# Performance work log

Measured on AMD Instinct MI355X. Metric: run time of the kernel, lower is better.

The kernel has to match this reference:

```python
import jax, jax.numpy as jnp
import numpy as np

FREQ = 129  # STFT_FILTERS // 2


def conv1d(x, w, b, stride, pad):
    # x: [B, Cin, L], w: [Cout, Cin, K] (torch Conv1d layout)
    out = jax.lax.conv_general_dilated(x, w, (stride,), [(pad, pad)],
                                       dimension_numbers=('NCH', 'OIH', 'NCH'))
    if b is not None:
        out = out + b[None, :, None]
    return out


def setup_inputs() -> dict:
    key = jax.random.key(0)
    ks = jax.random.split(key, 17)
    B = 16384
    s = 0.05
    return {
        'x': jax.random.normal(ks[0], (B, 512), jnp.float32),
        'state': jax.random.normal(ks[1], (2, B, 128), jnp.float32),
        'stft_w': jax.random.normal(ks[2], (258, 1, 256), jnp.float32) * s,
        'w1': jax.random.normal(ks[3], (128, 129, 3), jnp.float32) * s,
        'b1': jax.random.normal(ks[4], (128,), jnp.float32) * s,
        'w2': jax.random.normal(ks[5], (64, 128, 3), jnp.float32) * s,
        'b2': jax.random.normal(ks[6], (64,), jnp.float32) * s,
        'w3': jax.random.normal(ks[7], (64, 64, 3), jnp.float32) * s,
        'b3': jax.random.normal(ks[8], (64,), jnp.float32) * s,
        'w4': jax.random.normal(ks[9], (128, 64, 3), jnp.float32) * s,
        'b4': jax.random.normal(ks[10], (128,), jnp.float32) * s,
        'w_ih': jax.random.normal(ks[11], (512, 128), jnp.float32) * s,
        'w_hh': jax.random.normal(ks[12], (512, 128), jnp.float32) * s,
        'b_ih': jax.random.normal(ks[13], (512,), jnp.float32) * s,
        'b_hh': jax.random.normal(ks[14], (512,), jnp.float32) * s,
        'fw': jax.random.normal(ks[15], (1, 128, 1), jnp.float32) * s,
        'fb': jax.random.normal(ks[16], (1,), jnp.float32) * s,
    }


def reference(x, state, stft_w, w1, b1, w2, b2, w3, b3, w4, b4,
              w_ih, w_hh, b_ih, b_hh, fw, fb):
    # reflect-pad right by 64: [B, 512] -> [B, 576], add channel dim
    xp = jnp.pad(x, ((0, 0), (0, 64)), mode='reflect')[:, None, :]
    s = conv1d(xp, stft_w, None, 128, 0)            # [B, 258, 3]
    real, imag = s[:, :FREQ], s[:, FREQ:]
    h = jnp.sqrt(real * real + imag * imag)          # magnitude [B, 129, 3]
    h = jax.nn.relu(conv1d(h, w1, b1, 1, 1))         # [B, 128, 3]
    h = jax.nn.relu(conv1d(h, w2, b2, 2, 1))         # [B, 64, 2]
    h = jax.nn.relu(conv1d(h, w3, b3, 2, 1))         # [B, 64, 1]
    h = jax.nn.relu(conv1d(h, w4, b4, 1, 1))         # [B, 128, 1]
    feat = h[:, :, 0]                                # [B, 128]
    # torch LSTMCell: gate order i, f, g, o
    gates = feat @ w_ih.T + b_ih + state[0] @ w_hh.T + b_hh
    i, f, g, o = jnp.split(gates, 4, axis=1)
    c = jax.nn.sigmoid(f) * state[1] + jax.nn.sigmoid(i) * jnp.tanh(g)
    hn = jax.nn.sigmoid(o) * jnp.tanh(c)
    new_state = jnp.stack([hn, c], axis=0)           # [2, B, 128]
    z = jax.nn.relu(hn)[:, :, None]                  # [B, 128, 1]
    z = jax.nn.sigmoid(conv1d(z, fw, fb, 1, 0))      # [B, 1, 1]
    out = z[:, 0].mean(axis=1, keepdims=True)        # [B, 1]
    return out, new_state
```

## Files before the change

kernel.cpp:

```cpp
#include <hip/hip_runtime.h>
#include <math.h>

typedef unsigned short ushort_t;
typedef short short8 __attribute__((ext_vector_type(8)));
typedef float floatx4 __attribute__((ext_vector_type(4)));

#define MFMA16(a,b,c) __builtin_amdgcn_mfma_f32_16x16x32_bf16((a),(b),(c),0,0,0)

#define PK_STFT 0
#define PK_W1   69632
#define PK_W2   131072
#define PK_W3   155648
#define PK_W4   167936
#define PK_LSTM 176128
#define OFF_MAG 307200
#define OFF_FEAT 8171520

__device__ __forceinline__ ushort_t f2bf(float f){
    unsigned int u = __float_as_uint(f);
    u += 0x7fffu + ((u >> 16) & 1u);
    return (ushort_t)(u >> 16);
}
__device__ __forceinline__ float bf2f(ushort_t h){
    return __uint_as_float(((unsigned int)h) << 16);
}
__device__ __forceinline__ unsigned int pack2(float a, float b){
    return (unsigned int)f2bf(a) | ((unsigned int)f2bf(b) << 16);
}
__device__ __forceinline__ float sigf(float v){ return 1.f / (1.f + expf(-v)); }

__global__ __launch_bounds__(256) void prep_kernel(
    const float* __restrict__ stft_w, const float* __restrict__ w1,
    const float* __restrict__ w2, const float* __restrict__ w3,
    const float* __restrict__ w4, const float* __restrict__ wih,
    const float* __restrict__ whh, ushort_t* __restrict__ wp)
{
    int i = blockIdx.x * 256 + threadIdx.x;
    if (i >= 307200) return;
    float val = 0.f;
    if (i < PK_W1) {
        int frag = i >> 9, rr = i & 511, l = rr >> 3, j = rr & 7;
        int ct = frag >> 3, kk = frag & 7;
        int kd = kk * 32 + ((l >> 4) << 3) + j;
        int n = ct * 16 + (l & 15);
        val = (n < 258) ? stft_w[n * 256 + kd] : 0.f;
    } else if (i < PK_W2) {
        int r = i - PK_W1;
        int tap = r / 20480; r -= tap * 20480;
        int frag = r >> 9, rr = r & 511, l = rr >> 3, j = rr & 7;
        int ct = frag / 5, kk = frag - ct * 5;
        int kd = kk * 32 + ((l >> 4) << 3) + j;
        int c = ct * 16 + (l & 15);
        val = (kd < 129) ? w1[c * 387 + kd * 3 + tap] : 0.f;
    } else if (i < PK_W3) {
        int r = i - PK_W2;
        int frag = r >> 9, rr = r & 511, l = rr >> 3, j = rr & 7;
        int ct = frag / 12, kk = frag - ct * 12;
        int kd = kk * 32 + ((l >> 4) << 3) + j;
        int k = kd >> 7, f = kd & 127;
        int c = ct * 16 + (l & 15);
        val = w2[c * 384 + f * 3 + k];
    } else if (i < PK_W4) {
        int r = i - PK_W3;
        int frag = r >> 9, rr = r & 511, l = rr >> 3, j = rr & 7;
        int ct = frag / 6, kk = frag - ct * 6;
        int kd = kk * 32 + ((l >> 4) << 3) + j;
        int k = kd >> 6, f = kd & 63;
        int c = ct * 16 + (l & 15);
        val = w3[c * 192 + f * 3 + k];
    } else if (i < PK_LSTM) {
        int r = i - PK_W4;
        int frag = r >> 9, rr = r & 511, l = rr >> 3, j = rr & 7;
        int ct = frag >> 1, kk = frag & 1;
        int kd = kk * 32 + ((l >> 4) << 3) + j;
        int c = ct * 16 + (l & 15);
        val = w4[c * 192 + kd * 3 + 1];
    } else {
        int r = i - PK_LSTM;
        int frag = r >> 9, rr = r & 511, l = rr >> 3, j = rr & 7;
        int ct = frag >> 3, kk = frag & 7;
        int kd = kk * 32 + ((l >> 4) << 3) + j;
        int n = ct * 16 + (l & 15);
        val = (kd < 128) ? wih[n * 128 + kd] : whh[n * 128 + (kd - 128)];
    }
    wp[i] = f2bf(val);
}

__global__ __launch_bounds__(256) void stft_kernel(
    const float* __restrict__ x, const ushort_t* __restrict__ wp,
    ushort_t* __restrict__ magg)
{
    __shared__ ushort_t xs[48 * 264];
    __shared__ ushort_t s[48 * 264];
    const int tid = threadIdx.x, lane = tid & 63, wid = tid >> 6;
    const int l15 = lane & 15, lk = lane >> 4;

    {
        const float4* xg = (const float4*)(x + (size_t)blockIdx.x * 16 * 512);
#pragma unroll
        for (int i = 0; i < 8; ++i) {
            int idx4 = tid + i * 256;
            float4 v = xg[idx4];
            int b = idx4 >> 7, c4 = idx4 & 127;
            int si = c4 * 4, t1 = si >> 7;
            unsigned int u0 = pack2(v.x, v.y), u1 = pack2(v.z, v.w);
            if (t1 < 3) {
                ushort_t* p = &xs[(b * 3 + t1) * 264 + (si & 127)];
                *(unsigned int*)p = u0; *(unsigned int*)(p + 2) = u1;
            }
            if (t1 >= 1) {
                ushort_t* p = &xs[(b * 3 + t1 - 1) * 264 + (si & 127) + 128];
                *(unsigned int*)p = u0; *(unsigned int*)(p + 2) = u1;
            }
        }
    }
    __syncthreads();

    for (int ct = wid; ct < 17; ct += 4) {
        short8 bfrag[8];
        const short8* bp = (const short8*)(wp + PK_STFT) + (size_t)(ct * 8) * 64 + lane;
#pragma unroll
        for (int kk = 0; kk < 8; ++kk) bfrag[kk] = bp[kk * 64];
        int col = ct * 16 + l15;
#pragma unroll
        for (int rt = 0; rt < 3; ++rt) {
            const ushort_t* abase = &xs[(rt * 16 + l15) * 264 + lk * 8];
            floatx4 acc = {0.f, 0.f, 0.f, 0.f};
#pragma unroll
            for (int kk = 0; kk < 8; ++kk) {
                short8 af = *(const short8*)(abase + kk * 32);
                acc = MFMA16(af, bfrag[kk], acc);
            }
            if (col < 258) {
                int r0 = rt * 16 + lk * 4;
#pragma unroll
                for (int jj = 0; jj < 4; ++jj) s[(r0 + jj) * 264 + col] = f2bf(acc[jj]);
            }
        }
    }
    __syncthreads();

    {
        size_t ob = (size_t)blockIdx.x * 16 * 480;
        for (int idx = tid; idx < 48 * 129; idx += 256) {
            int bt = idx / 129, f = idx - bt * 129;
            float re = bf2f(s[bt * 264 + f]);
            float im = bf2f(s[bt * 264 + 129 + f]);
            int b = bt / 3, t = bt - b * 3;
            magg[ob + b * 480 + t * 160 + f] = f2bf(sqrtf(re * re + im * im));
        }
        for (int idx = tid; idx < 48 * 31; idx += 256) {
            int bt = idx / 31, f = 129 + (idx - bt * 31);
            int b = bt / 3, t = bt - b * 3;
            magg[ob + b * 480 + t * 160 + f] = 0;
        }
    }
}

__global__ __launch_bounds__(256) void conv_kernel(
    const ushort_t* __restrict__ wp, const ushort_t* __restrict__ magg,
    const float* __restrict__ b1, const float* __restrict__ b2,
    const float* __restrict__ b3, const float* __restrict__ b4,
    ushort_t* __restrict__ featg)
{
    __shared__ ushort_t big[26880];
    __shared__ ushort_t h2h[32 * 3 * 72];
    __shared__ ushort_t h3s[32 * 72];
    const int tid = threadIdx.x, lane = tid & 63, wid = tid >> 6;
    const int l15 = lane & 15, lk = lane >> 4;

    {
        unsigned int* bz = (unsigned int*)big;
        for (int i = tid; i < 5376; i += 256) {
            int bb = i / 168, r = i - bb * 168;
            int tp = (r < 84) ? 0 : 4, f2 = (r < 84) ? r : r - 84;
            bz[(bb * 5 + tp) * 84 + f2] = 0u;
        }
        for (int i = tid; i < 32 * 36; i += 256) {
            int bb = i / 36, f2 = i - bb * 36;
            ((unsigned int*)h2h)[bb * 108 + f2] = 0u;
        }
        const unsigned int* mg = (const unsigned int*)(magg + (size_t)blockIdx.x * 32 * 480);
        for (int i = tid; i < 7680; i += 256) {
            int bb = i / 240, r = i - bb * 240;
            int t = r / 80, f2 = r - t * 80;
            bz[(bb * 5 + 1 + t) * 84 + f2] = mg[i];
        }
    }
    __syncthreads();

    floatx4 acc1[2][6];
#pragma unroll
    for (int ci = 0; ci < 2; ++ci)
#pragma unroll
        for (int rt = 0; rt < 6; ++rt) acc1[ci][rt] = (floatx4){0.f, 0.f, 0.f, 0.f};
#pragma unroll
    for (int ci = 0; ci < 2; ++ci) {
        int ct = wid + ci * 4;
        short8 bfrag[15];
#pragma unroll
        for (int tap = 0; tap < 3; ++tap)
#pragma unroll
            for (int kk = 0; kk < 5; ++kk)
                bfrag[tap * 5 + kk] = ((const short8*)(wp + PK_W1))[(size_t)(tap * 40 + ct * 5 + kk) * 64 + lane];
#pragma unroll
        for (int rt = 0; rt < 6; ++rt) {
            int obt = rt * 16 + l15;
            int b = obt / 3, t = obt - b * 3;
#pragma unroll
            for (int tap = 0; tap < 3; ++tap) {
                const ushort_t* abase = &big[(b * 5 + t + tap) * 168 + lk * 8];
#pragma unroll
                for (int kk = 0; kk < 5; ++kk) {
                    short8 af = *(const short8*)(abase + kk * 32);
                    acc1[ci][rt] = MFMA16(af, bfrag[tap * 5 + kk], acc1[ci][rt]);
                }
            }
        }
    }
    __syncthreads();

    {
        unsigned int* h1z = (unsigned int*)big;
        for (int i = tid; i < 32 * 136; i += 256) {
            int bb = i / 136, r = i - bb * 136;
            int tp = (r < 68) ? 0 : 4, f2 = (r < 68) ? r : r - 68;
            h1z[(bb * 5 + tp) * 68 + f2] = 0u;
        }
#pragma unroll
        for (int ci = 0; ci < 2; ++ci) {
            int ct = wid + ci * 4;
            int col = ct * 16 + l15;
            float bias = b1[col];
#pragma unroll
            for (int rt = 0; rt < 6; ++rt)
#pragma unroll
                for (int jj = 0; jj < 4; ++jj) {
                    int obt = rt * 16 + lk * 4 + jj;
                    int b = obt / 3, t = obt - b * 3;
                    big[(b * 5 + t + 1) * 136 + col] = f2bf(fmaxf(acc1[ci][rt][jj] + bias, 0.f));
                }
        }
    }
    __syncthreads();

    {
        int ct = wid;
        short8 bfrag[12];
#pragma unroll
        for (int kk = 0; kk < 12; ++kk)
            bfrag[kk] = ((const short8*)(wp + PK_W2))[(size_t)(ct * 12 + kk) * 64 + lane];
        int col = ct * 16 + l15;
        float bias = b2[col];
#pragma unroll
        for (int rt = 0; rt < 4; ++rt) {
            floatx4 acc = {0.f, 0.f, 0.f, 0.f};
            int orow = rt * 16 + l15;
            int b = orow >> 1, t2 = orow & 1;
#pragma unroll
            for (int kk = 0; kk < 12; ++kk) {
                int k = kk >> 2, f = (kk & 3) * 32 + lk * 8;
                short8 af = *(const short8*)(&big[(b * 5 + 2 * t2 + k) * 136 + f]);
                acc = MFMA16(af, bfrag[kk], acc);
            }
#pragma unroll
            for (int jj = 0; jj < 4; ++jj) {
                int orw = rt * 16 + lk * 4 + jj;
                int bb = orw >> 1, tt = orw & 1;
                h2h[(bb * 3 + 1 + tt) * 72 + col] = f2bf(fmaxf(acc[jj] + bias, 0.f));
            }
        }
    }
    __syncthreads();

    {
        int ct = wid;
        short8 bfrag[6];
#pragma unroll
        for (int kk = 0; kk < 6; ++kk)
            bfrag[kk] = ((const short8*)(wp + PK_W3))[(size_t)(ct * 6 + kk) * 64 + lane];
        int col = ct * 16 + l15;
        float bias = b3[col];
#pragma unroll
        for (int rt = 0; rt < 2; ++rt) {
            floatx4 acc = {0.f, 0.f, 0.f, 0.f};
            int b = rt * 16 + l15;
#pragma unroll
            for (int kk = 0; kk < 6; ++kk) {
                int k = kk >> 1, f = (kk & 1) * 32 + lk * 8;
                short8 af = *(const short8*)(&h2h[(b * 3 + k) * 72 + f]);
                acc = MFMA16(af, bfrag[kk], acc);
            }
#pragma unroll
            for (int jj = 0; jj < 4; ++jj) {
                int bb = rt * 16 + lk * 4 + jj;
                h3s[bb * 72 + col] = f2bf(fmaxf(acc[jj] + bias, 0.f));
            }
        }
    }
    __syncthreads();

    {
#pragma unroll
        for (int ci = 0; ci < 2; ++ci) {
            int ct = wid + ci * 4;
            short8 bf0 = ((const short8*)(wp + PK_W4))[(size_t)(ct * 2 + 0) * 64 + lane];
            short8 bf1 = ((const short8*)(wp + PK_W4))[(size_t)(ct * 2 + 1) * 64 + lane];
            int col = ct * 16 + l15;
            float bias = b4[col];
#pragma unroll
            for (int rt = 0; rt < 2; ++rt) {
                floatx4 acc = {0.f, 0.f, 0.f, 0.f};
                int b = rt * 16 + l15;
                short8 a0 = *(const short8*)(&h3s[b * 72 + lk * 8]);
                short8 a1 = *(const short8*)(&h3s[b * 72 + 32 + lk * 8]);
                acc = MFMA16(a0, bf0, acc);
                acc = MFMA16(a1, bf1, acc);
#pragma unroll
                for (int jj = 0; jj < 4; ++jj) {
                    int bb = rt * 16 + lk * 4 + jj;
                    featg[((size_t)blockIdx.x * 32 + bb) * 128 + col] = f2bf(fmaxf(acc[jj] + bias, 0.f));
                }
            }
        }
    }
}

__global__ __launch_bounds__(256) void lstm_kernel(
    const ushort_t* __restrict__ featg, const float* __restrict__ state,
    const ushort_t* __restrict__ wp, const float* __restrict__ bih,
    const float* __restrict__ bhh, const float* __restrict__ fw,
    const float* __restrict__ fbp, float* __restrict__ out, int B)
{
    __shared__ ushort_t inc[32 * 264];
    __shared__ float red[128];
    const int tid = threadIdx.x, lane = tid & 63, wid = tid >> 6;
    const int l15 = lane & 15, lk = lane >> 4;
    const size_t b0 = (size_t)blockIdx.x * 32;

    {
        const unsigned int* fg = (const unsigned int*)(featg + b0 * 128);
        unsigned int* ip = (unsigned int*)inc;
        for (int i = tid; i < 2048; i += 256) {
            int bb = i >> 6, f2 = i & 63;
            ip[bb * 132 + f2] = fg[i];
        }
        const float* hp = state + b0 * 128;
        for (int i = tid; i < 2048; i += 256) {
            int bb = i >> 6, c2 = i & 63;
            float2 v = *(const float2*)&hp[bb * 128 + c2 * 2];
            ip[bb * 132 + 64 + c2] = pack2(v.x, v.y);
        }
    }
    __syncthreads();

    floatx4 acc[8][2];
#pragma unroll
    for (int ci = 0; ci < 8; ++ci) {
        int ct = wid + ci * 4;
        short8 bfrag[8];
#pragma unroll
        for (int kk = 0; kk < 8; ++kk)
            bfrag[kk] = ((const short8*)(wp + PK_LSTM))[(size_t)(ct * 8 + kk) * 64 + lane];
#pragma unroll
        for (int rt = 0; rt < 2; ++rt) {
            const ushort_t* abase = &inc[(rt * 16 + l15) * 264 + lk * 8];
            floatx4 a = {0.f, 0.f, 0.f, 0.f};
#pragma unroll
            for (int kk = 0; kk < 8; ++kk) {
                short8 af = *(const short8*)(abase + kk * 32);
                a = MFMA16(af, bfrag[kk], a);
            }
            acc[ci][rt] = a;
        }
    }

    const float* cprev = state + (size_t)B * 128;
    float* outh = out + B;
    float* outc = out + B + (size_t)B * 128;
    float ph[2][4];
#pragma unroll
    for (int rt = 0; rt < 2; ++rt)
#pragma unroll
        for (int jj = 0; jj < 4; ++jj) ph[rt][jj] = 0.f;

#pragma unroll
    for (int g2 = 0; g2 < 2; ++g2) {
        int cc = (wid + g2 * 4) * 16 + l15;
        float bi = bih[cc] + bhh[cc];
        float bf_ = bih[cc + 128] + bhh[cc + 128];
        float bg = bih[cc + 256] + bhh[cc + 256];
        float bo = bih[cc + 384] + bhh[cc + 384];
        float fwv = fw[cc];
#pragma unroll
        for (int rt = 0; rt < 2; ++rt)
#pragma unroll
            for (int jj = 0; jj < 4; ++jj) {
                int row = rt * 16 + lk * 4 + jj;
                size_t gb = b0 + row;
                float gi = acc[g2][rt][jj] + bi;
                float gf = acc[g2 + 2][rt][jj] + bf_;
                float gg = acc[g2 + 4][rt][jj] + bg;
                float go = acc[g2 + 6][rt][jj] + bo;
                float cp = cprev[gb * 128 + cc];
                float cn = sigf(gf) * cp + sigf(gi) * tanhf(gg);
                float hn = sigf(go) * tanhf(cn);
                outh[gb * 128 + cc] = hn;
                outc[gb * 128 + cc] = cn;
                ph[rt][jj] += fmaxf(hn, 0.f) * fwv;
            }
    }

#pragma unroll
    for (int rt = 0; rt < 2; ++rt)
#pragma unroll
        for (int jj = 0; jj < 4; ++jj) {
            float v = ph[rt][jj];
            v += __shfl_xor(v, 1, 64);
            v += __shfl_xor(v, 2, 64);
            v += __shfl_xor(v, 4, 64);
            v += __shfl_xor(v, 8, 64);
            if (l15 == 0) red[wid * 32 + rt * 16 + lk * 4 + jj] = v;
        }
    __syncthreads();
    if (tid < 32) {
        float v = red[tid] + red[32 + tid] + red[64 + tid] + red[96 + tid];
        out[b0 + tid] = sigf(v + fbp[0]);
    }
}

extern "C" void kernel_launch(void* const* d_in, const int* in_sizes, int n_in,
                              void* d_out, int out_size, void* d_ws, size_t ws_size,
                              hipStream_t stream) {
    const float* x      = (const float*)d_in[0];
    const float* state  = (const float*)d_in[1];
    const float* stft_w = (const float*)d_in[2];
    const float* w1     = (const float*)d_in[3];
    const float* b1     = (const float*)d_in[4];
    const float* w2     = (const float*)d_in[5];
    const float* b2     = (const float*)d_in[6];
    const float* w3     = (const float*)d_in[7];
    const float* b3     = (const float*)d_in[8];
    const float* w4     = (const float*)d_in[9];
    const float* b4     = (const float*)d_in[10];
    const float* wih    = (const float*)d_in[11];
    const float* whh    = (const float*)d_in[12];
    const float* bih    = (const float*)d_in[13];
    const float* bhh    = (const float*)d_in[14];
    const float* fw     = (const float*)d_in[15];
    const float* fbp    = (const float*)d_in[16];

    ushort_t* wp = (ushort_t*)d_ws;
    const int B = in_sizes[0] / 512;

    prep_kernel<<<1200, 256, 0, stream>>>(stft_w, w1, w2, w3, w4, wih, whh, wp);
    stft_kernel<<<B / 16, 256, 0, stream>>>(x, wp, wp + OFF_MAG);
    conv_kernel<<<B / 32, 256, 0, stream>>>(wp, wp + OFF_MAG, b1, b2, b3, b4, wp + OFF_FEAT);
    lstm_kernel<<<B / 32, 256, 0, stream>>>(wp + OFF_FEAT, state, wp, bih, bhh, fw, fbp,
                                            (float*)d_out, B);
}
```

Measured before the change: 83.77 us.

## Halve conv tile to 16 rows, widen LSTM blocks to 8 waves, use fast sigmoid/tanh

The conv kernel now processes 16 batch rows per block instead of 32, doubling grid size and halving LDS and register accumulators to raise occupancy. The LSTM kernel moves to 512 threads so each wave owns one 16-column slice across all four gates, and the previous cell state is prefetched before the GEMM. Sigmoid and tanh use hardware exp2/rcp intrinsics instead of expf/tanhf. The trade-off is more blocks with redundant weight-fragment loads per block, plus slightly lower accuracy from the approximate transcendentals.

After: 73.69 us. -12.0%, faster.

```diff
diff --git a/kernel.cpp b/kernel.cpp
--- a/kernel.cpp
+++ b/kernel.cpp
@@ -27,7 +27,12 @@
 __device__ __forceinline__ unsigned int pack2(float a, float b){
     return (unsigned int)f2bf(a) | ((unsigned int)f2bf(b) << 16);
 }
-__device__ __forceinline__ float sigf(float v){ return 1.f / (1.f + expf(-v)); }
+__device__ __forceinline__ float fsig(float v){
+    return __builtin_amdgcn_rcpf(1.f + __builtin_amdgcn_exp2f(-1.44269504f * v));
+}
+__device__ __forceinline__ float ftanh(float v){
+    return 2.f * __builtin_amdgcn_rcpf(1.f + __builtin_amdgcn_exp2f(-2.88539008f * v)) - 1.f;
+}
 
 __global__ __launch_bounds__(256) void prep_kernel(
     const float* __restrict__ stft_w, const float* __restrict__ w1,
@@ -163,25 +168,25 @@
     const float* __restrict__ b3, const float* __restrict__ b4,
     ushort_t* __restrict__ featg)
 {
-    __shared__ ushort_t big[26880];
-    __shared__ ushort_t h2h[32 * 3 * 72];
-    __shared__ ushort_t h3s[32 * 72];
+    __shared__ ushort_t big[13440];
+    __shared__ ushort_t h2h[16 * 3 * 72];
+    __shared__ ushort_t h3s[16 * 72];
     const int tid = threadIdx.x, lane = tid & 63, wid = tid >> 6;
     const int l15 = lane & 15, lk = lane >> 4;
 
     {
         unsigned int* bz = (unsigned int*)big;
-        for (int i = tid; i < 5376; i += 256) {
+        for (int i = tid; i < 2688; i += 256) {
             int bb = i / 168, r = i - bb * 168;
             int tp = (r < 84) ? 0 : 4, f2 = (r < 84) ? r : r - 84;
             bz[(bb * 5 + tp) * 84 + f2] = 0u;
         }
-        for (int i = tid; i < 32 * 36; i += 256) {
+        for (int i = tid; i < 576; i += 256) {
             int bb = i / 36, f2 = i - bb * 36;
             ((unsigned int*)h2h)[bb * 108 + f2] = 0u;
         }
-        const unsigned int* mg = (const unsigned int*)(magg + (size_t)blockIdx.x * 32 * 480);
-        for (int i = tid; i < 7680; i += 256) {
+        const unsigned int* mg = (const unsigned int*)(magg + (size_t)blockIdx.x * 16 * 480);
+        for (int i = tid; i < 3840; i += 256) {
             int bb = i / 240, r = i - bb * 240;
             int t = r / 80, f2 = r - t * 80;
             bz[(bb * 5 + 1 + t) * 84 + f2] = mg[i];
@@ -189,11 +194,11 @@
     }
     __syncthreads();
 
-    floatx4 acc1[2][6];
+    floatx4 acc1[2][3];
 #pragma unroll
     for (int ci = 0; ci < 2; ++ci)
 #pragma unroll
-        for (int rt = 0; rt < 6; ++rt) acc1[ci][rt] = (floatx4){0.f, 0.f, 0.f, 0.f};
+        for (int rt = 0; rt < 3; ++rt) acc1[ci][rt] = (floatx4){0.f, 0.f, 0.f, 0.f};
 #pragma unroll
     for (int ci = 0; ci < 2; ++ci) {
         int ct = wid + ci * 4;
@@ -204,7 +209,7 @@
             for (int kk = 0; kk < 5; ++kk)
                 bfrag[tap * 5 + kk] = ((const short8*)(wp + PK_W1))[(size_t)(tap * 40 + ct * 5 + kk) * 64 + lane];
 #pragma unroll
-        for (int rt = 0; rt < 6; ++rt) {
+        for (int rt = 0; rt < 3; ++rt) {
             int obt = rt * 16 + l15;
             int b = obt / 3, t = obt - b * 3;
 #pragma unroll
@@ -222,7 +227,7 @@
 
     {
         unsigned int* h1z = (unsigned int*)big;
-        for (int i = tid; i < 32 * 136; i += 256) {
+        for (int i = tid; i < 2176; i += 256) {
             int bb = i / 136, r = i - bb * 136;
             int tp = (r < 68) ? 0 : 4, f2 = (r < 68) ? r : r - 68;
             h1z[(bb * 5 + tp) * 68 + f2] = 0u;
@@ -233,7 +238,7 @@
             int col = ct * 16 + l15;
             float bias = b1[col];
 #pragma unroll
-            for (int rt = 0; rt < 6; ++rt)
+            for (int rt = 0; rt < 3; ++rt)
 #pragma unroll
                 for (int jj = 0; jj < 4; ++jj) {
                     int obt = rt * 16 + lk * 4 + jj;
@@ -253,7 +258,7 @@
         int col = ct * 16 + l15;
         float bias = b2[col];
 #pragma unroll
-        for (int rt = 0; rt < 4; ++rt) {
+        for (int rt = 0; rt < 2; ++rt) {
             floatx4 acc = {0.f, 0.f, 0.f, 0.f};
             int orow = rt * 16 + l15;
             int b = orow >> 1, t2 = orow & 1;
@@ -281,21 +286,18 @@
             bfrag[kk] = ((const short8*)(wp + PK_W3))[(size_t)(ct * 6 + kk) * 64 + lane];
         int col = ct * 16 + l15;
         float bias = b3[col];
-#pragma unroll
-        for (int rt = 0; rt < 2; ++rt) {
-            floatx4 acc = {0.f, 0.f, 0.f, 0.f};
-            int b = rt * 16 + l15;
-#pragma unroll
-            for (int kk = 0; kk < 6; ++kk) {
-                int k = kk >> 1, f = (kk & 1) * 32 + lk * 8;
-                short8 af = *(const short8*)(&h2h[(b * 3 + k) * 72 + f]);
-                acc = MFMA16(af, bfrag[kk], acc);
-            }
-#pragma unroll
-            for (int jj = 0; jj < 4; ++jj) {
-                int bb = rt * 16 + lk * 4 + jj;
-                h3s[bb * 72 + col] = f2bf(fmaxf(acc[jj] + bias, 0.f));
-            }
+        floatx4 acc = {0.f, 0.f, 0.f, 0.f};
+        int b = l15;
+#pragma unroll
+        for (int kk = 0; kk < 6; ++kk) {
+            int k = kk >> 1, f = (kk & 1) * 32 + lk * 8;
+            short8 af = *(const short8*)(&h2h[(b * 3 + k) * 72 + f]);
+            acc = MFMA16(af, bfrag[kk], acc);
+        }
+#pragma unroll
+        for (int jj = 0; jj < 4; ++jj) {
+            int bb = lk * 4 + jj;
+            h3s[bb * 72 + col] = f2bf(fmaxf(acc[jj] + bias, 0.f));
         }
     }
     __syncthreads();
@@ -308,45 +310,51 @@
             short8 bf1 = ((const short8*)(wp + PK_W4))[(size_t)(ct * 2 + 1) * 64 + lane];
             int col = ct * 16 + l15;
             float bias = b4[col];
-#pragma unroll
-            for (int rt = 0; rt < 2; ++rt) {
-                floatx4 acc = {0.f, 0.f, 0.f, 0.f};
-                int b = rt * 16 + l15;
-                short8 a0 = *(const short8*)(&h3s[b * 72 + lk * 8]);
-                short8 a1 = *(const short8*)(&h3s[b * 72 + 32 + lk * 8]);
-                acc = MFMA16(a0, bf0, acc);
-                acc = MFMA16(a1, bf1, acc);
-#pragma unroll
-                for (int jj = 0; jj < 4; ++jj) {
-                    int bb = rt * 16 + lk * 4 + jj;
-                    featg[((size_t)blockIdx.x * 32 + bb) * 128 + col] = f2bf(fmaxf(acc[jj] + bias, 0.f));
-                }
-            }
-        }
-    }
-}
-
-__global__ __launch_bounds__(256) void lstm_kernel(
+            floatx4 acc = {0.f, 0.f, 0.f, 0.f};
+            int b = l15;
+            short8 a0 = *(const short8*)(&h3s[b * 72 + lk * 8]);
+            short8 a1 = *(const short8*)(&h3s[b * 72 + 32 + lk * 8]);
+            acc = MFMA16(a0, bf0, acc);
+            acc = MFMA16(a1, bf1, acc);
+#pragma unroll
+            for (int jj = 0; jj < 4; ++jj) {
+                int bb = lk * 4 + jj;
+                featg[((size_t)blockIdx.x * 16 + bb) * 128 + col] = f2bf(fmaxf(acc[jj] + bias, 0.f));
+            }
+        }
+    }
+}
+
+__global__ __launch_bounds__(512) void lstm_kernel(
     const ushort_t* __restrict__ featg, const float* __restrict__ state,
     const ushort_t* __restrict__ wp, const float* __restrict__ bih,
     const float* __restrict__ bhh, const float* __restrict__ fw,
     const float* __restrict__ fbp, float* __restrict__ out, int B)
 {
     __shared__ ushort_t inc[32 * 264];
-    __shared__ float red[128];
+    __shared__ float red[256];
     const int tid = threadIdx.x, lane = tid & 63, wid = tid >> 6;
     const int l15 = lane & 15, lk = lane >> 4;
     const size_t b0 = (size_t)blockIdx.x * 32;
+    const int cc = wid * 16 + l15;
+
+    const float* cprev = state + (size_t)B * 128;
+    float cpv[2][4];
+#pragma unroll
+    for (int rt = 0; rt < 2; ++rt)
+#pragma unroll
+        for (int jj = 0; jj < 4; ++jj)
+            cpv[rt][jj] = cprev[(b0 + rt * 16 + lk * 4 + jj) * 128 + cc];
 
     {
         const unsigned int* fg = (const unsigned int*)(featg + b0 * 128);
         unsigned int* ip = (unsigned int*)inc;
-        for (int i = tid; i < 2048; i += 256) {
+        for (int i = tid; i < 2048; i += 512) {
             int bb = i >> 6, f2 = i & 63;
             ip[bb * 132 + f2] = fg[i];
         }
         const float* hp = state + b0 * 128;
-        for (int i = tid; i < 2048; i += 256) {
+        for (int i = tid; i < 2048; i += 512) {
             int bb = i >> 6, c2 = i & 63;
             float2 v = *(const float2*)&hp[bb * 128 + c2 * 2];
             ip[bb * 132 + 64 + c2] = pack2(v.x, v.y);
@@ -354,10 +362,10 @@
     }
     __syncthreads();
 
-    floatx4 acc[8][2];
-#pragma unroll
-    for (int ci = 0; ci < 8; ++ci) {
-        int ct = wid + ci * 4;
+    floatx4 acc[4][2];
+#pragma unroll
+    for (int ci = 0; ci < 4; ++ci) {
+        int ct = wid + ci * 8;
         short8 bfrag[8];
 #pragma unroll
         for (int kk = 0; kk < 8; ++kk)
@@ -375,41 +383,30 @@
         }
     }
 
-    const float* cprev = state + (size_t)B * 128;
     float* outh = out + B;
     float* outc = out + B + (size_t)B * 128;
     float ph[2][4];
+    const float bi = bih[cc] + bhh[cc];
+    const float bf_ = bih[cc + 128] + bhh[cc + 128];
+    const float bg = bih[cc + 256] + bhh[cc + 256];
+    const float bo = bih[cc + 384] + bhh[cc + 384];
+    const float fwv = fw[cc];
 #pragma unroll
     for (int rt = 0; rt < 2; ++rt)
 #pragma unroll
-        for (int jj = 0; jj < 4; ++jj) ph[rt][jj] = 0.f;
-
-#pragma unroll
-    for (int g2 = 0; g2 < 2; ++g2) {
-        int cc = (wid + g2 * 4) * 16 + l15;
-        float bi = bih[cc] + bhh[cc];
-        float bf_ = bih[cc + 128] + bhh[cc + 128];
-        float bg = bih[cc + 256] + bhh[cc + 256];
-        float bo = bih[cc + 384] + bhh[cc + 384];
-        float fwv = fw[cc];
-#pragma unroll
-        for (int rt = 0; rt < 2; ++rt)
-#pragma unroll
-            for (int jj = 0; jj < 4; ++jj) {
-                int row = rt * 16 + lk * 4 + jj;
-                size_t gb = b0 + row;
-                float gi = acc[g2][rt][jj] + bi;
-                float gf = acc[g2 + 2][rt][jj] + bf_;
-                float gg = acc[g2 + 4][rt][jj] + bg;
-                float go = acc[g2 + 6][rt][jj] + bo;
-                float cp = cprev[gb * 128 + cc];
-                float cn = sigf(gf) * cp + sigf(gi) * tanhf(gg);
-                float hn = sigf(go) * tanhf(cn);
-                outh[gb * 128 + cc] = hn;
-                outc[gb * 128 + cc] = cn;
-                ph[rt][jj] += fmaxf(hn, 0.f) * fwv;
-            }
-    }
+        for (int jj = 0; jj < 4; ++jj) {
+            int row = rt * 16 + lk * 4 + jj;
+            size_t gb = b0 + row;
+            float gi = acc[0][rt][jj] + bi;
+            float gf = acc[1][rt][jj] + bf_;
+            float gg = acc[2][rt][jj] + bg;
+            float go = acc[3][rt][jj] + bo;
+            float cn = fsig(gf) * cpv[rt][jj] + fsig(gi) * ftanh(gg);
+            float hn = fsig(go) * ftanh(cn);
+            outh[gb * 128 + cc] = hn;
+            outc[gb * 128 + cc] = cn;
+            ph[rt][jj] = fmaxf(hn, 0.f) * fwv;
+        }
 
 #pragma unroll
     for (int rt = 0; rt < 2; ++rt)
@@ -424,8 +421,10 @@
         }
     __syncthreads();
     if (tid < 32) {
-        float v = red[tid] + red[32 + tid] + red[64 + tid] + red[96 + tid];
-        out[b0 + tid] = sigf(v + fbp[0]);
+        float v = 0.f;
+#pragma unroll
+        for (int w = 0; w < 8; ++w) v += red[w * 32 + tid];
+        out[b0 + tid] = fsig(v + fbp[0]);
     }
 }
 
@@ -455,7 +454,7 @@
 
     prep_kernel<<<1200, 256, 0, stream>>>(stft_w, w1, w2, w3, w4, wih, whh, wp);
     stft_kernel<<<B / 16, 256, 0, stream>>>(x, wp, wp + OFF_MAG);
-    conv_kernel<<<B / 32, 256, 0, stream>>>(wp, wp + OFF_MAG, b1, b2, b3, b4, wp + OFF_FEAT);
-    lstm_kernel<<<B / 32, 256, 0, stream>>>(wp + OFF_FEAT, state, wp, bih, bhh, fw, fbp,
+    conv_kernel<<<B / 16, 256, 0, stream>>>(wp, wp + OFF_MAG, b1, b2, b3, b4, wp + OFF_FEAT);
+    lstm_kernel<<<B / 32, 512, 0, stream>>>(wp + OFF_FEAT, state, wp, bih, bhh, fw, fbp,
                                             (float*)d_out, B);
 }
```
